# Optimization experiments

Hardware: AMD Instinct MI355X
Metric: run time of the kernel (lower is better)

The kernel has to match this reference:

```python
import jax, jax.numpy as jnp
import numpy as np

N_NODES = 50000
N_EDGES = 800000
N_FEAT = 256
HIDDEN = 64
N_CLASSES = 16
T_END = 3.0  # opt['time']; rk4 takes one step over [0, 3]


def spline_conv(x, src, dst, p, W, R, b, n):
    """SplineConv, dim=1, kernel_size=2, degree=1 open B-spline, aggr='mean'.
    x: [n, Cin]; src/dst: [E]; p: [E,1] pseudo-coords in [0,1];
    W: [2, Cin, Cout]; R: [Cin, Cout]; b: [Cout]."""
    xj = x[src]  # gather source node features [E, Cin]
    # basis weights for K=2, degree=1: (1-p) on kernel 0, p on kernel 1
    msg = ((1.0 - p) * xj) @ W[0] + (p * xj) @ W[1]  # [E, Cout]
    agg = jax.ops.segment_sum(msg, dst, num_segments=n)
    deg = jax.ops.segment_sum(jnp.ones((msg.shape[0], 1), msg.dtype), dst, num_segments=n)
    return agg / jnp.maximum(deg, 1.0) + x @ R + b


def setup_inputs() -> dict:
    key = jax.random.key(0)
    ks = jax.random.split(key, 20)
    x = jax.random.normal(ks[0], (N_NODES, N_FEAT), jnp.float32)
    edge_attr = jax.random.uniform(ks[1], (N_EDGES, 1), jnp.float32)
    src = jax.random.randint(ks[2], (N_EDGES,), 0, N_NODES)
    dst = jax.random.randint(ks[3], (N_EDGES,), 0, N_NODES)

    def w(k, shape, fan_in):
        s = 1.0 / np.sqrt(fan_in)
        return jax.random.uniform(k, shape, jnp.float32, -s, s)

    # conv1: num_features -> hidden
    W1 = w(ks[4], (2, N_FEAT, HIDDEN), N_FEAT)
    R1 = w(ks[5], (N_FEAT, HIDDEN), N_FEAT)
    b1 = jnp.zeros((HIDDEN,), jnp.float32)
    # ODE func: two stacked SplineConvs hidden -> hidden
    Wa = w(ks[6], (2, HIDDEN, HIDDEN), HIDDEN)
    Ra = w(ks[7], (HIDDEN, HIDDEN), HIDDEN)
    ba = jnp.zeros((HIDDEN,), jnp.float32)
    Wb = w(ks[8], (2, HIDDEN, HIDDEN), HIDDEN)
    Rb = w(ks[9], (HIDDEN, HIDDEN), HIDDEN)
    bb = jnp.zeros((HIDDEN,), jnp.float32)
    # conv2: hidden -> num_classes
    W2 = w(ks[10], (2, HIDDEN, N_CLASSES), HIDDEN)
    R2 = w(ks[11], (HIDDEN, N_CLASSES), HIDDEN)
    b2 = jnp.zeros((N_CLASSES,), jnp.float32)

    return dict(x=x, edge_attr=edge_attr, src=src, dst=dst,
                W1=W1, R1=R1, b1=b1, Wa=Wa, Ra=Ra, ba=ba,
                Wb=Wb, Rb=Rb, bb=bb, W2=W2, R2=R2, b2=b2)


def reference(x, edge_attr, src, dst, W1, R1, b1, Wa, Ra, ba, Wb, Rb, bb, W2, R2, b2):
    n = x.shape[0]
    p = edge_attr
    h = jnp.tanh(spline_conv(x, src, dst, p, W1, R1, b1, n))
    # dropout is identity in eval mode

    def f(y):  # GCNLayer: two stacked SplineConvs, no activation
        y = spline_conv(y, src, dst, p, Wa, Ra, ba, n)
        return spline_conv(y, src, dst, p, Wb, Rb, bb, n)

    # single RK4 step from t=0 to t=T_END (torchdiffeq fixed-grid rk4 on s_span=[0,3])
    k1 = f(h)
    k2 = f(h + 0.5 * T_END * k1)
    k3 = f(h + 0.5 * T_END * k2)
    k4 = f(h + T_END * k3)
    h = h + (T_END / 6.0) * (k1 + 2.0 * k2 + 2.0 * k3 + k4)

    out = jnp.tanh(spline_conv(h, src, dst, p, W2, R2, b2, n))
    return jax.nn.log_softmax(out, axis=1)
```

## Files before the change

kernel.cpp:

```cpp
#include <hip/hip_runtime.h>
#include <math.h>

static inline int ceil_div(int a, int b) { return (a + b - 1) / b; }


__global__ __launch_bounds__(256) void zero2(int* __restrict__ a, int* __restrict__ b,
                                             int n) {
    int i = blockIdx.x * 256 + threadIdx.x;
    if (i < n) { a[i] = 0; b[i] = 0; }
}

__global__ __launch_bounds__(256) void hist_kernel(const int* __restrict__ dst,
                                                   int* __restrict__ deg, int E) {
    int e = blockIdx.x * 256 + threadIdx.x;
    if (e < E) atomicAdd(&deg[dst[e]], 1);
}

__global__ __launch_bounds__(256) void scan_blocksum(const int* __restrict__ deg,
                                                     int* __restrict__ bsum, int n) {
    __shared__ int red[256];
    int t = threadIdx.x;
    int base = blockIdx.x * 2048 + t * 8;
    int s = 0;
    #pragma unroll
    for (int i = 0; i < 8; ++i) {
        int idx = base + i;
        if (idx < n) s += deg[idx];
    }
    red[t] = s;
    __syncthreads();
    #pragma unroll
    for (int off = 128; off >= 1; off >>= 1) {
        if (t < off) red[t] += red[t + off];
        __syncthreads();
    }
    if (t == 0) bsum[blockIdx.x] = red[0];
}

__global__ __launch_bounds__(256) void scan_tops(int* __restrict__ bsum, int nb) {
    __shared__ int sh[256];
    int t = threadIdx.x;
    int orig = (t < nb) ? bsum[t] : 0;
    sh[t] = orig;
    __syncthreads();
    for (int off = 1; off < 256; off <<= 1) {
        int add = (t >= off) ? sh[t - off] : 0;
        __syncthreads();
        sh[t] += add;
        __syncthreads();
    }
    if (t < nb) bsum[t] = sh[t] - orig;
}

__global__ __launch_bounds__(256) void scan_final(const int* __restrict__ deg,
                                                  const int* __restrict__ bsum,
                                                  int* __restrict__ rowp,
                                                  float* __restrict__ invd,
                                                  int n, int E) {
    __shared__ int sh[256];
    int t = threadIdx.x;
    int base = blockIdx.x * 2048 + t * 8;
    int loc[8];
    int s = 0;
    #pragma unroll
    for (int i = 0; i < 8; ++i) {
        int idx = base + i;
        int d = (idx < n) ? deg[idx] : 0;
        loc[i] = d;
        s += d;
    }
    sh[t] = s;
    __syncthreads();
    for (int off = 1; off < 256; off <<= 1) {
        int add = (t >= off) ? sh[t - off] : 0;
        __syncthreads();
        sh[t] += add;
        __syncthreads();
    }
    int run = bsum[blockIdx.x] + (sh[t] - s);
    #pragma unroll
    for (int i = 0; i < 8; ++i) {
        int idx = base + i;
        if (idx < n) {
            rowp[idx] = run;
            int d = loc[i];
            run += d;
            invd[idx] = 1.0f / (float)(d > 1 ? d : 1);
        }
    }
    if (blockIdx.x == 0 && t == 0) rowp[n] = E;
}

__global__ __launch_bounds__(256) void scatter_idx(const int* __restrict__ dst,
                                                   const int* __restrict__ rowp,
                                                   int* __restrict__ fill,
                                                   int* __restrict__ ei, int E) {
    int e = blockIdx.x * 256 + threadIdx.x;
    if (e >= E) return;
    int d = dst[e];
    int pos = rowp[d] + atomicAdd(&fill[d], 1);
    ei[pos] = e;
}

__global__ __launch_bounds__(256) void sort_fill(const int* __restrict__ rowp,
                                                 int* __restrict__ ei,
                                                 const int* __restrict__ src,
                                                 const float* __restrict__ p,
                                                 int* __restrict__ es,
                                                 float* __restrict__ ep, int n) {
    int node = blockIdx.x * 256 + threadIdx.x;
    if (node >= n) return;
    int b = rowp[node], e = rowp[node + 1];
    for (int i = b + 1; i < e; ++i) {
        int key = ei[i];
        int j = i - 1;
        while (j >= b && ei[j] > key) { ei[j + 1] = ei[j]; --j; }
        ei[j + 1] = key;
    }
    for (int i = b; i < e; ++i) {
        int id = ei[i];
        es[i] = src[id];
        ep[i] = p[id];
    }
}

__global__ __launch_bounds__(256) void pack_all(
    const float* __restrict__ W1, const float* __restrict__ R1,
    const float* __restrict__ Wa, const float* __restrict__ Ra,
    const float* __restrict__ Wb, const float* __restrict__ Rb,
    const float* __restrict__ W2, const float* __restrict__ R2,
    float* __restrict__ Bc1, float* __restrict__ Bca,
    float* __restrict__ Bcb, float* __restrict__ Bc2) {
    int idx = blockIdx.x * 256 + threadIdx.x;
    const int S1 = 256 * 192, S2 = 192 * 64, S4 = 64 * 48;
    if (idx < S1) {
        int k = idx / 192, c = idx % 192;
        float v;
        if (c < 64)       v = W1[k * 64 + c];
        else if (c < 128) v = W1[256 * 64 + k * 64 + (c - 64)];
        else              v = R1[k * 64 + (c - 128)];
        Bc1[idx] = v;
        return;
    }
    idx -= S1;
    if (idx < S2) { Bca[idx] = (idx < 8192) ? Wa[idx] : Ra[idx - 8192]; return; }
    idx -= S2;
    if (idx < S2) { Bcb[idx] = (idx < 8192) ? Wb[idx] : Rb[idx - 8192]; return; }
    idx -= S2;
    if (idx < S4) {
        int k = idx / 48, c = idx % 48;
        float v;
        if (c < 16)      v = W2[k * 16 + c];
        else if (c < 32) v = W2[64 * 16 + k * 16 + (c - 16)];
        else             v = R2[k * 16 + (c - 32)];
        Bc2[idx] = v;
    }
}

__global__ __launch_bounds__(256) void edge_agg64_v4(const float* __restrict__ x,
                                                     const int* __restrict__ rowp,
                                                     const int* __restrict__ es,
                                                     const float* __restrict__ ep,
                                                     const float* __restrict__ invd,
                                                     float* __restrict__ agg, int n) {
    int gid = blockIdx.x * 256 + threadIdx.x;
    int node = gid >> 4;
    if (node >= n) return;
    int c4 = (gid & 15) << 2;
    int e = rowp[node], eend = rowp[node + 1];
    float sx = 0.f, sy = 0.f, sz = 0.f, sw = 0.f;
    float px = 0.f, py = 0.f, pz = 0.f, pw = 0.f;
    for (; e + 4 <= eend; e += 4) {
        int s0 = es[e], s1 = es[e + 1], s2 = es[e + 2], s3 = es[e + 3];
        float p0 = ep[e], p1 = ep[e + 1], p2 = ep[e + 2], p3 = ep[e + 3];
        float4 v0 = *reinterpret_cast<const float4*>(&x[(size_t)s0 * 64 + c4]);
        float4 v1 = *reinterpret_cast<const float4*>(&x[(size_t)s1 * 64 + c4]);
        float4 v2 = *reinterpret_cast<const float4*>(&x[(size_t)s2 * 64 + c4]);
        float4 v3 = *reinterpret_cast<const float4*>(&x[(size_t)s3 * 64 + c4]);
        sx += (v0.x + v1.x) + (v2.x + v3.x);
        sy += (v0.y + v1.y) + (v2.y + v3.y);
        sz += (v0.z + v1.z) + (v2.z + v3.z);
        sw += (v0.w + v1.w) + (v2.w + v3.w);
        px = fmaf(p0, v0.x, fmaf(p1, v1.x, fmaf(p2, v2.x, fmaf(p3, v3.x, px))));
        py = fmaf(p0, v0.y, fmaf(p1, v1.y, fmaf(p2, v2.y, fmaf(p3, v3.y, py))));
        pz = fmaf(p0, v0.z, fmaf(p1, v1.z, fmaf(p2, v2.z, fmaf(p3, v3.z, pz))));
        pw = fmaf(p0, v0.w, fmaf(p1, v1.w, fmaf(p2, v2.w, fmaf(p3, v3.w, pw))));
    }
    for (; e < eend; ++e) {
        int s = es[e];
        float pe = ep[e];
        float4 v = *reinterpret_cast<const float4*>(&x[(size_t)s * 64 + c4]);
        sx += v.x; sy += v.y; sz += v.z; sw += v.w;
        px = fmaf(pe, v.x, px); py = fmaf(pe, v.y, py);
        pz = fmaf(pe, v.z, pz); pw = fmaf(pe, v.w, pw);
    }
    float w = invd[node];
    float4 a0 = make_float4((sx - px) * w, (sy - py) * w, (sz - pz) * w, (sw - pw) * w);
    float4 a1 = make_float4(px * w, py * w, pz * w, pw * w);
    *reinterpret_cast<float4*>(&agg[(size_t)node * 128 + c4]) = a0;
    *reinterpret_cast<float4*>(&agg[(size_t)node * 128 + 64 + c4]) = a1;
}

__global__ __launch_bounds__(256) void hidden_gemm_db(
    const float* __restrict__ agg, const float* __restrict__ in,
    const float* __restrict__ B, const float* __restrict__ bias,
    int n, int mode, float* __restrict__ u_out,
    const float* __restrict__ hbuf, const float* __restrict__ acc_in,
    float* __restrict__ acc_out, float* __restrict__ t_out,
    float c1, float c2, float c3) {
    __shared__ __align__(16) float As[2][16][68];
    __shared__ __align__(16) float Bs[2][16][68];
    const int t = threadIdx.x;
    const int row0 = blockIdx.x * 64;
    const int ty = t >> 4, tx = t & 15;
    const int lrow = t >> 2, lk = (t & 3) << 2;
    const int bkk = t >> 4, bcol = (t & 15) << 2;

    float4 av = make_float4(0.f, 0.f, 0.f, 0.f);
    {
        int r = row0 + lrow;
        if (r < n) av = *reinterpret_cast<const float4*>(&agg[(size_t)r * 128 + lk]);
    }
    float4 bv = *reinterpret_cast<const float4*>(&B[(size_t)bkk * 64 + bcol]);
    As[0][lk + 0][lrow] = av.x; As[0][lk + 1][lrow] = av.y;
    As[0][lk + 2][lrow] = av.z; As[0][lk + 3][lrow] = av.w;
    *reinterpret_cast<float4*>(&Bs[0][bkk][bcol]) = bv;
    __syncthreads();

    float acc[4][4];
    #pragma unroll
    for (int i = 0; i < 4; ++i)
        #pragma unroll
        for (int j = 0; j < 4; ++j) acc[i][j] = 0.f;

    for (int kt = 0; kt < 12; ++kt) {
        const int cur = kt & 1;
        if (kt + 1 < 12) {
            int k0 = (kt + 1) << 4;
            int r = row0 + lrow;
            int kk = k0 + lk;
            av = make_float4(0.f, 0.f, 0.f, 0.f);
            if (r < n)
                av = (kk < 128)
                    ? *reinterpret_cast<const float4*>(&agg[(size_t)r * 128 + kk])
                    : *reinterpret_cast<const float4*>(&in[(size_t)r * 64 + (kk - 128)]);
            bv = *reinterpret_cast<const float4*>(&B[(size_t)(k0 + bkk) * 64 + bcol]);
        }
        #pragma unroll
        for (int kk = 0; kk < 16; ++kk) {
            float4 a4 = *reinterpret_cast<const float4*>(&As[cur][kk][ty << 2]);
            float4 b4 = *reinterpret_cast<const float4*>(&Bs[cur][kk][tx << 2]);
            float aa[4] = {a4.x, a4.y, a4.z, a4.w};
            float bb[4] = {b4.x, b4.y, b4.z, b4.w};
            #pragma unroll
            for (int i = 0; i < 4; ++i)
                #pragma unroll
                for (int j = 0; j < 4; ++j)
                    acc[i][j] = fmaf(aa[i], bb[j], acc[i][j]);
        }
        if (kt + 1 < 12) {
            const int nx = cur ^ 1;
            As[nx][lk + 0][lrow] = av.x; As[nx][lk + 1][lrow] = av.y;
            As[nx][lk + 2][lrow] = av.z; As[nx][lk + 3][lrow] = av.w;
            *reinterpret_cast<float4*>(&Bs[nx][bkk][bcol]) = bv;
        }
        __syncthreads();
    }

    float4 bia = *reinterpret_cast<const float4*>(&bias[tx << 2]);
    #pragma unroll
    for (int i = 0; i < 4; ++i) {
        int r = row0 + (ty << 2) + i;
        if (r >= n) continue;
        size_t idx = (size_t)r * 64 + (tx << 2);
        float4 v = make_float4(acc[i][0] + bia.x, acc[i][1] + bia.y,
                               acc[i][2] + bia.z, acc[i][3] + bia.w);
        if (mode == 0) {
            *reinterpret_cast<float4*>(&u_out[idx]) = v;
        } else {
            float4 ai = make_float4(0.f, 0.f, 0.f, 0.f);
            if (acc_in) ai = *reinterpret_cast<const float4*>(&acc_in[idx]);
            float4 an = make_float4(ai.x + c3 * v.x, ai.y + c3 * v.y,
                                    ai.z + c3 * v.z, ai.w + c3 * v.w);
            *reinterpret_cast<float4*>(&acc_out[idx]) = an;
            float4 hb = *reinterpret_cast<const float4*>(&hbuf[idx]);
            float4 to = make_float4(hb.x + c1 * v.x + c2 * an.x,
                                    hb.y + c1 * v.y + c2 * an.y,
                                    hb.z + c1 * v.z + c2 * an.z,
                                    hb.w + c1 * v.w + c2 * an.w);
            *reinterpret_cast<float4*>(&t_out[idx]) = to;
        }
    }
}

__global__ __launch_bounds__(128) void conv1_gemm_v3(const float* __restrict__ x,
                                                     const float* __restrict__ B,
                                                     int n, float* __restrict__ yz,
                                                     float* __restrict__ base,
                                                     const float* __restrict__ b1) {
    __shared__ __align__(16) float As[16][68];
    __shared__ __align__(16) float Bs[16][200];
    const int t = threadIdx.x;
    const int row0 = blockIdx.x * 64;
    const int ty = t >> 4, tx = t & 15;
    const int bkk0 = t >> 4, bcol = (t & 15) << 2;
    float acc[8][12];
    #pragma unroll
    for (int i = 0; i < 8; ++i)
        #pragma unroll
        for (int j = 0; j < 12; ++j) acc[i][j] = 0.f;

    for (int kt = 0; kt < 16; ++kt) {
        int k0 = kt << 4;
        #pragma unroll
        for (int hh = 0; hh < 2; ++hh) {
            int q = t + 128 * hh;
            int row = q >> 2;
            int lkq = (q & 3) << 2;
            float4 av = make_float4(0.f, 0.f, 0.f, 0.f);
            int r = row0 + row;
            if (r < n)
                av = *reinterpret_cast<const float4*>(&x[(size_t)r * 256 + k0 + lkq]);
            As[lkq + 0][row] = av.x; As[lkq + 1][row] = av.y;
            As[lkq + 2][row] = av.z; As[lkq + 3][row] = av.w;
        }
        #pragma unroll
        for (int hh = 0; hh < 2; ++hh) {
            int kk = bkk0 + 8 * hh;
            const float* bp = &B[(size_t)(k0 + kk) * 192 + bcol];
            *reinterpret_cast<float4*>(&Bs[kk][bcol])       = *reinterpret_cast<const float4*>(bp);
            *reinterpret_cast<float4*>(&Bs[kk][bcol + 64])  = *reinterpret_cast<const float4*>(bp + 64);
            *reinterpret_cast<float4*>(&Bs[kk][bcol + 128]) = *reinterpret_cast<const float4*>(bp + 128);
        }
        __syncthreads();
        #pragma unroll
        for (int kk = 0; kk < 16; ++kk) {
            float4 a0 = *reinterpret_cast<const float4*>(&As[kk][ty << 3]);
            float4 a1 = *reinterpret_cast<const float4*>(&As[kk][(ty << 3) + 4]);
            float4 b0 = *reinterpret_cast<const float4*>(&Bs[kk][tx << 2]);
            float4 b1q = *reinterpret_cast<const float4*>(&Bs[kk][(tx << 2) + 64]);
            float4 b2q = *reinterpret_cast<const float4*>(&Bs[kk][(tx << 2) + 128]);
            float aa[8] = {a0.x, a0.y, a0.z, a0.w, a1.x, a1.y, a1.z, a1.w};
            float bb[12] = {b0.x, b0.y, b0.z, b0.w, b1q.x, b1q.y, b1q.z, b1q.w,
                            b2q.x, b2q.y, b2q.z, b2q.w};
            #pragma unroll
            for (int i = 0; i < 8; ++i)
                #pragma unroll
                for (int j = 0; j < 12; ++j)
                    acc[i][j] = fmaf(aa[i], bb[j], acc[i][j]);
        }
        __syncthreads();
    }

    float4 bb4 = *reinterpret_cast<const float4*>(&b1[tx << 2]);
    #pragma unroll
    for (int i = 0; i < 8; ++i) {
        int r = row0 + (ty << 3) + i;
        if (r >= n) continue;
        float4 q0 = make_float4(acc[i][0], acc[i][1], acc[i][2], acc[i][3]);
        float4 q1 = make_float4(acc[i][4], acc[i][5], acc[i][6], acc[i][7]);
        float4 q2 = make_float4(acc[i][8] + bb4.x, acc[i][9] + bb4.y,
                                acc[i][10] + bb4.z, acc[i][11] + bb4.w);
        *reinterpret_cast<float4*>(&yz[(size_t)r * 128 + (tx << 2)]) = q0;
        *reinterpret_cast<float4*>(&yz[(size_t)r * 128 + 64 + (tx << 2)]) = q1;
        *reinterpret_cast<float4*>(&base[(size_t)r * 64 + (tx << 2)]) = q2;
    }
}

__global__ __launch_bounds__(256) void edge_tf64_v8(const float* __restrict__ yz,
                                                    const int* __restrict__ rowp,
                                                    const int* __restrict__ es,
                                                    const float* __restrict__ ep,
                                                    const float* __restrict__ invd,
                                                    const float* __restrict__ base,
                                                    float* __restrict__ out, int n) {
    int gid = blockIdx.x * 256 + threadIdx.x;
    int node = gid >> 3;
    if (node >= n) return;
    int c8 = (gid & 7) << 3;
    int e = rowp[node], eend = rowp[node + 1];
    float a[8] = {0.f, 0.f, 0.f, 0.f, 0.f, 0.f, 0.f, 0.f};
    for (; e + 2 <= eend; e += 2) {
        int s0 = es[e], s1 = es[e + 1];
        float p0 = ep[e], p1 = ep[e + 1];
        float4 y0a = *reinterpret_cast<const float4*>(&yz[(size_t)s0 * 128 + c8]);
        float4 y0b = *reinterpret_cast<const float4*>(&yz[(size_t)s0 * 128 + c8 + 4]);
        float4 z0a = *reinterpret_cast<const float4*>(&yz[(size_t)s0 * 128 + 64 + c8]);
        float4 z0b = *reinterpret_cast<const float4*>(&yz[(size_t)s0 * 128 + 64 + c8 + 4]);
        float4 y1a = *reinterpret_cast<const float4*>(&yz[(size_t)s1 * 128 + c8]);
        float4 y1b = *reinterpret_cast<const float4*>(&yz[(size_t)s1 * 128 + c8 + 4]);
        float4 z1a = *reinterpret_cast<const float4*>(&yz[(size_t)s1 * 128 + 64 + c8]);
        float4 z1b = *reinterpret_cast<const float4*>(&yz[(size_t)s1 * 128 + 64 + c8 + 4]);
        const float* ya0 = &y0a.x; const float* yb0 = &y0b.x;
        const float* za0 = &z0a.x; const float* zb0 = &z0b.x;
        const float* ya1 = &y1a.x; const float* yb1 = &y1b.x;
        const float* za1 = &z1a.x; const float* zb1 = &z1b.x;
        #pragma unroll
        for (int j = 0; j < 4; ++j) {
            a[j]     += fmaf(p0, za0[j] - ya0[j], ya0[j]) + fmaf(p1, za1[j] - ya1[j], ya1[j]);
            a[4 + j] += fmaf(p0, zb0[j] - yb0[j], yb0[j]) + fmaf(p1, zb1[j] - yb1[j], yb1[j]);
        }
    }
    for (; e < eend; ++e) {
        int s = es[e];
        float pe = ep[e];
        float4 ya = *reinterpret_cast<const float4*>(&yz[(size_t)s * 128 + c8]);
        float4 yb = *reinterpret_cast<const float4*>(&yz[(size_t)s * 128 + c8 + 4]);
        float4 za = *reinterpret_cast<const float4*>(&yz[(size_t)s * 128 + 64 + c8]);
        float4 zb = *reinterpret_cast<const float4*>(&yz[(size_t)s * 128 + 64 + c8 + 4]);
        const float* fy = &ya.x; const float* gy = &yb.x;
        const float* fz = &za.x; const float* gz = &zb.x;
        #pragma unroll
        for (int j = 0; j < 4; ++j) {
            a[j]     += fmaf(pe, fz[j] - fy[j], fy[j]);
            a[4 + j] += fmaf(pe, gz[j] - gy[j], gy[j]);
        }
    }
    float w = invd[node];
    size_t idx = (size_t)node * 64 + c8;
    float4 ba = *reinterpret_cast<const float4*>(&base[idx]);
    float4 bbv = *reinterpret_cast<const float4*>(&base[idx + 4]);
    float4 o0 = make_float4(tanhf(fmaf(a[0], w, ba.x)), tanhf(fmaf(a[1], w, ba.y)),
                            tanhf(fmaf(a[2], w, ba.z)), tanhf(fmaf(a[3], w, ba.w)));
    float4 o1 = make_float4(tanhf(fmaf(a[4], w, bbv.x)), tanhf(fmaf(a[5], w, bbv.y)),
                            tanhf(fmaf(a[6], w, bbv.z)), tanhf(fmaf(a[7], w, bbv.w)));
    *reinterpret_cast<float4*>(&out[idx]) = o0;
    *reinterpret_cast<float4*>(&out[idx + 4]) = o1;
}

__global__ __launch_bounds__(256) void edge_tf16_lsm(const float* __restrict__ yz,
                                                     const int* __restrict__ rowp,
                                                     const int* __restrict__ es,
                                                     const float* __restrict__ ep,
                                                     const float* __restrict__ invd,
                                                     const float* __restrict__ base,
                                                     float* __restrict__ out, int n) {
    int gid = blockIdx.x * 256 + threadIdx.x;
    int node = gid >> 4;
    if (node >= n) return;
    int c = gid & 15;
    int e = rowp[node], eend = rowp[node + 1];
    float a = 0.f;
    for (; e + 4 <= eend; e += 4) {
        int s0 = es[e], s1 = es[e + 1], s2 = es[e + 2], s3 = es[e + 3];
        float p0 = ep[e], p1 = ep[e + 1], p2 = ep[e + 2], p3 = ep[e + 3];
        float y0 = yz[(size_t)s0 * 32 + c],      z0 = yz[(size_t)s0 * 32 + 16 + c];
        float y1 = yz[(size_t)s1 * 32 + c],      z1 = yz[(size_t)s1 * 32 + 16 + c];
        float y2 = yz[(size_t)s2 * 32 + c],      z2 = yz[(size_t)s2 * 32 + 16 + c];
        float y3 = yz[(size_t)s3 * 32 + c],      z3 = yz[(size_t)s3 * 32 + 16 + c];
        a += fmaf(p0, z0 - y0, y0);
        a += fmaf(p1, z1 - y1, y1);
        a += fmaf(p2, z2 - y2, y2);
        a += fmaf(p3, z3 - y3, y3);
    }
    for (; e < eend; ++e) {
        int s = es[e]; float pe = ep[e];
        float y = yz[(size_t)s * 32 + c], z = yz[(size_t)s * 32 + 16 + c];
        a += fmaf(pe, z - y, y);
    }
    float o = tanhf(a * invd[node] + base[(size_t)node * 16 + c]);
    float m = o;
    #pragma unroll
    for (int off = 8; off >= 1; off >>= 1) m = fmaxf(m, __shfl_xor(m, off, 16));
    float ex = expf(o - m);
    float s = ex;
    #pragma unroll
    for (int off = 8; off >= 1; off >>= 1) s += __shfl_xor(s, off, 16);
    out[(size_t)node * 16 + c] = (o - m) - logf(s);
}

__global__ __launch_bounds__(256) void gemm_tiled(
    const float* __restrict__ A0, int lda0, int K0,
    const float* __restrict__ A1, int lda1,
    const float* __restrict__ B,
    int n, int K, int M,
    float* __restrict__ out0, int w0, const float* __restrict__ bias0,
    float* __restrict__ out1, int w1, const float* __restrict__ bias1,
    int split) {
    __shared__ __align__(16) float As[16][68];
    __shared__ __align__(16) float Bs[16][68];
    const int t = threadIdx.x;
    const int row0 = blockIdx.x * 64;
    const int col0 = blockIdx.y * 64;
    const int ty = t >> 4, tx = t & 15;
    const int lrow = t >> 2, lk = (t & 3) << 2;
    const int bkk = t >> 4, bcol = (t & 15) << 2;
    float acc[4][4];
    #pragma unroll
    for (int i = 0; i < 4; ++i)
        #pragma unroll
        for (int j = 0; j < 4; ++j) acc[i][j] = 0.f;

    for (int k0 = 0; k0 < K; k0 += 16) {
        float4 av = make_float4(0.f, 0.f, 0.f, 0.f);
        {
            int r = row0 + lrow;
            if (r < n) {
                int kk = k0 + lk;
                const float* src = (kk < K0)
                    ? (A0 + (size_t)r * lda0 + kk)
                    : (A1 + (size_t)r * lda1 + (kk - K0));
                av = *reinterpret_cast<const float4*>(src);
            }
        }
        float4 bv = make_float4(0.f, 0.f, 0.f, 0.f);
        {
            int c = col0 + bcol;
            int kk = k0 + bkk;
            if (c < M) bv = *reinterpret_cast<const float4*>(B + (size_t)kk * M + c);
        }
        As[lk + 0][lrow] = av.x; As[lk + 1][lrow] = av.y;
        As[lk + 2][lrow] = av.z; As[lk + 3][lrow] = av.w;
        *reinterpret_cast<float4*>(&Bs[bkk][bcol]) = bv;
        __syncthreads();
        #pragma unroll
        for (int kk = 0; kk < 16; ++kk) {
            float4 a4 = *reinterpret_cast<const float4*>(&As[kk][ty << 2]);
            float4 b4 = *reinterpret_cast<const float4*>(&Bs[kk][tx << 2]);
            float aa[4] = {a4.x, a4.y, a4.z, a4.w};
            float bb[4] = {b4.x, b4.y, b4.z, b4.w};
            #pragma unroll
            for (int i = 0; i < 4; ++i)
                #pragma unroll
                for (int j = 0; j < 4; ++j)
                    acc[i][j] = fmaf(aa[i], bb[j], acc[i][j]);
        }
        __syncthreads();
    }

    #pragma unroll
    for (int i = 0; i < 4; ++i) {
        int r = row0 + (ty << 2) + i;
        if (r >= n) continue;
        #pragma unroll
        for (int j = 0; j < 4; ++j) {
            int c = col0 + (tx << 2) + j;
            if (c >= M) continue;
            float v = acc[i][j];
            if (c < split) {
                if (bias0) v += bias0[c];
                out0[(size_t)r * w0 + c] = v;
            } else {
                int cc = c - split;
                if (bias1) v += bias1[cc];
                out1[(size_t)r * w1 + cc] = v;
            }
        }
    }
}


static void hidden_conv(hipStream_t stream, const float* in, float* agg,
                        const int* rowp, const int* es, const float* ep,
                        const float* invd, const float* Bc, const float* bias, int n,
                        int mode, float* u_out,
                        const float* h, const float* acc_in, float* acc_out,
                        float* t_out, float c1, float c2, float c3) {
    edge_agg64_v4<<<ceil_div(n * 16, 256), 256, 0, stream>>>(in, rowp, es, ep, invd,
                                                             agg, n);
    hidden_gemm_db<<<ceil_div(n, 64), 256, 0, stream>>>(agg, in, Bc, bias, n, mode,
                                                        u_out, h, acc_in, acc_out,
                                                        t_out, c1, c2, c3);
}

extern "C" void kernel_launch(void* const* d_in, const int* in_sizes, int n_in,
                              void* d_out, int out_size, void* d_ws, size_t ws_size,
                              hipStream_t stream) {
    const float* x  = (const float*)d_in[0];
    const float* pE = (const float*)d_in[1];
    const int*   sr = (const int*)d_in[2];
    const int*   ds = (const int*)d_in[3];
    const float* W1 = (const float*)d_in[4];
    const float* R1 = (const float*)d_in[5];
    const float* b1 = (const float*)d_in[6];
    const float* Wa = (const float*)d_in[7];
    const float* Ra = (const float*)d_in[8];
    const float* ba = (const float*)d_in[9];
    const float* Wb = (const float*)d_in[10];
    const float* Rb = (const float*)d_in[11];
    const float* bb = (const float*)d_in[12];
    const float* W2 = (const float*)d_in[13];
    const float* R2 = (const float*)d_in[14];
    const float* b2 = (const float*)d_in[15];
    const int n = in_sizes[0] / 256;
    const int E = in_sizes[2];
    float* out = (float*)d_out;

    char* w = (char*)d_ws;
    auto alloc = [&](size_t bytes) -> void* {
        void* ptr = (void*)w;
        w += (bytes + 255) & ~(size_t)255;
        return ptr;
    };
    int nscan = ceil_div(n, 2048);
    int*   deg  = (int*)alloc((size_t)n * 4);
    int*   fill = (int*)alloc((size_t)n * 4);
    int*   rowp = (int*)alloc((size_t)(n + 1) * 4);
    float* invd = (float*)alloc((size_t)n * 4);
    int*   bsum = (int*)alloc((size_t)256 * 4);
    int*   ei   = (int*)alloc((size_t)E * 4);
    int*   es   = (int*)alloc((size_t)E * 4);
    float* ep   = (float*)alloc((size_t)E * 4);
    float* Bc1  = (float*)alloc((size_t)256 * 192 * 4);
    float* Bca  = (float*)alloc((size_t)192 * 64 * 4);
    float* Bcb  = (float*)alloc((size_t)192 * 64 * 4);
    float* Bc2  = (float*)alloc((size_t)64 * 48 * 4);
    float* big0 = (float*)alloc((size_t)n * 128 * 4);
    float* big1 = (float*)alloc((size_t)n * 64 * 4);
    float* h    = (float*)alloc((size_t)n * 64 * 4);
    float* u    = (float*)alloc((size_t)n * 64 * 4);
    float* tb   = (float*)alloc((size_t)n * 64 * 4);
    float* acc  = (float*)alloc((size_t)n * 64 * 4);

    const int PACK_TOTAL = 256 * 192 + 2 * 192 * 64 + 64 * 48;

    zero2<<<ceil_div(n, 256), 256, 0, stream>>>(deg, fill, n);
    pack_all<<<ceil_div(PACK_TOTAL, 256), 256, 0, stream>>>(W1, R1, Wa, Ra, Wb, Rb,
                                                            W2, R2, Bc1, Bca, Bcb, Bc2);
    hist_kernel<<<ceil_div(E, 256), 256, 0, stream>>>(ds, deg, E);
    scan_blocksum<<<nscan, 256, 0, stream>>>(deg, bsum, n);
    scan_tops<<<1, 256, 0, stream>>>(bsum, nscan);
    scan_final<<<nscan, 256, 0, stream>>>(deg, bsum, rowp, invd, n, E);
    scatter_idx<<<ceil_div(E, 256), 256, 0, stream>>>(ds, rowp, fill, ei, E);
    sort_fill<<<ceil_div(n, 256), 256, 0, stream>>>(rowp, ei, sr, pE, es, ep, n);

    conv1_gemm_v3<<<ceil_div(n, 64), 128, 0, stream>>>(x, Bc1, n, big0, big1, b1);
    edge_tf64_v8<<<ceil_div(n * 8, 256), 256, 0, stream>>>(big0, rowp, es, ep, invd,
                                                           big1, h, n);

    hidden_conv(stream, h, big0, rowp, es, ep, invd, Bca, ba, n, 0, u,
                nullptr, nullptr, nullptr, nullptr, 0.f, 0.f, 0.f);
    hidden_conv(stream, u, big0, rowp, es, ep, invd, Bcb, bb, n, 1, nullptr,
                h, nullptr, acc, tb, 1.5f, 0.f, 1.f);
    hidden_conv(stream, tb, big0, rowp, es, ep, invd, Bca, ba, n, 0, u,
                nullptr, nullptr, nullptr, nullptr, 0.f, 0.f, 0.f);
    hidden_conv(stream, u, big0, rowp, es, ep, invd, Bcb, bb, n, 1, nullptr,
                h, acc, acc, tb, 1.5f, 0.f, 2.f);
    hidden_conv(stream, tb, big0, rowp, es, ep, invd, Bca, ba, n, 0, u,
                nullptr, nullptr, nullptr, nullptr, 0.f, 0.f, 0.f);
    hidden_conv(stream, u, big0, rowp, es, ep, invd, Bcb, bb, n, 1, nullptr,
                h, acc, acc, tb, 3.f, 0.f, 2.f);
    hidden_conv(stream, tb, big0, rowp, es, ep, invd, Bca, ba, n, 0, u,
                nullptr, nullptr, nullptr, nullptr, 0.f, 0.f, 0.f);
    hidden_conv(stream, u, big0, rowp, es, ep, invd, Bcb, bb, n, 1, nullptr,
                h, acc, acc, tb, 0.f, 0.5f, 1.f);

    gemm_tiled<<<dim3(ceil_div(n, 64), 1), 256, 0, stream>>>(
        tb, 64, 64, nullptr, 0, Bc2, n, 64, 48,
        big0, 32, nullptr, big1, 16, b2, 32);
    edge_tf16_lsm<<<ceil_div(n * 16, 256), 256, 0, stream>>>(big0, rowp, es, ep, invd,
                                                             big1, out, n);
}
```

Measured before the change: 878.9 us.

## Fuse setup kernels, deepen edge-gather unrolling, and retile conv1 GEMM for more threads

Merges the zeroing and weight-packing kernels into one grid-stride launch to save a launch. Adds deeper unrolled paths (8 edges, or 4 for the 128-wide gather) to the edge aggregation kernels so more independent gather loads are in flight. Changes the conv1 GEMM from 128 threads with 8x12 register tiles to 256 threads with 4x12 tiles, cutting per-thread registers to raise occupancy at the cost of less register reuse per thread.

```diff
diff --git a/kernel.cpp b/kernel.cpp
--- a/kernel.cpp
+++ b/kernel.cpp
@@ -4,10 +4,42 @@
 static inline int ceil_div(int a, int b) { return (a + b - 1) / b; }
 
 
-__global__ __launch_bounds__(256) void zero2(int* __restrict__ a, int* __restrict__ b,
-                                             int n) {
-    int i = blockIdx.x * 256 + threadIdx.x;
-    if (i < n) { a[i] = 0; b[i] = 0; }
+__global__ __launch_bounds__(256) void setup_zero_pack(
+    int* __restrict__ deg, int* __restrict__ fill, int n,
+    const float* __restrict__ W1, const float* __restrict__ R1,
+    const float* __restrict__ Wa, const float* __restrict__ Ra,
+    const float* __restrict__ Wb, const float* __restrict__ Rb,
+    const float* __restrict__ W2, const float* __restrict__ R2,
+    float* __restrict__ Bc1, float* __restrict__ Bca,
+    float* __restrict__ Bcb, float* __restrict__ Bc2) {
+    int gid = blockIdx.x * 256 + threadIdx.x;
+    int gstride = gridDim.x * 256;
+    for (int i = gid; i < n; i += gstride) { deg[i] = 0; fill[i] = 0; }
+    const int S1 = 256 * 192, S2 = 192 * 64, S4 = 64 * 48;
+    const int TOT = S1 + 2 * S2 + S4;
+    for (int i0 = gid; i0 < TOT; i0 += gstride) {
+        int idx = i0;
+        if (idx < S1) {
+            int k = idx / 192, c = idx % 192;
+            float v;
+            if (c < 64)       v = W1[k * 64 + c];
+            else if (c < 128) v = W1[256 * 64 + k * 64 + (c - 64)];
+            else              v = R1[k * 64 + (c - 128)];
+            Bc1[idx] = v;
+            continue;
+        }
+        idx -= S1;
+        if (idx < S2) { Bca[idx] = (idx < 8192) ? Wa[idx] : Ra[idx - 8192]; continue; }
+        idx -= S2;
+        if (idx < S2) { Bcb[idx] = (idx < 8192) ? Wb[idx] : Rb[idx - 8192]; continue; }
+        idx -= S2;
+        int k = idx / 48, c = idx % 48;
+        float v;
+        if (c < 16)      v = W2[k * 16 + c];
+        else if (c < 32) v = W2[64 * 16 + k * 16 + (c - 16)];
+        else             v = R2[k * 16 + (c - 32)];
+        Bc2[idx] = v;
+    }
 }
 
 __global__ __launch_bounds__(256) void hist_kernel(const int* __restrict__ dst,
@@ -124,40 +156,7 @@
     }
 }
 
-__global__ __launch_bounds__(256) void pack_all(
-    const float* __restrict__ W1, const float* __restrict__ R1,
-    const float* __restrict__ Wa, const float* __restrict__ Ra,
-    const float* __restrict__ Wb, const float* __restrict__ Rb,
-    const float* __restrict__ W2, const float* __restrict__ R2,
-    float* __restrict__ Bc1, float* __restrict__ Bca,
-    float* __restrict__ Bcb, float* __restrict__ Bc2) {
-    int idx = blockIdx.x * 256 + threadIdx.x;
-    const int S1 = 256 * 192, S2 = 192 * 64, S4 = 64 * 48;
-    if (idx < S1) {
-        int k = idx / 192, c = idx % 192;
-        float v;
-        if (c < 64)       v = W1[k * 64 + c];
-        else if (c < 128) v = W1[256 * 64 + k * 64 + (c - 64)];
-        else              v = R1[k * 64 + (c - 128)];
-        Bc1[idx] = v;
-        return;
-    }
-    idx -= S1;
-    if (idx < S2) { Bca[idx] = (idx < 8192) ? Wa[idx] : Ra[idx - 8192]; return; }
-    idx -= S2;
-    if (idx < S2) { Bcb[idx] = (idx < 8192) ? Wb[idx] : Rb[idx - 8192]; return; }
-    idx -= S2;
-    if (idx < S4) {
-        int k = idx / 48, c = idx % 48;
-        float v;
-        if (c < 16)      v = W2[k * 16 + c];
-        else if (c < 32) v = W2[64 * 16 + k * 16 + (c - 16)];
-        else             v = R2[k * 16 + (c - 32)];
-        Bc2[idx] = v;
-    }
-}
-
-__global__ __launch_bounds__(256) void edge_agg64_v4(const float* __restrict__ x,
+__global__ __launch_bounds__(256) void edge_agg64_u8(const float* __restrict__ x,
                                                      const int* __restrict__ rowp,
                                                      const int* __restrict__ es,
                                                      const float* __restrict__ ep,
@@ -170,6 +169,36 @@
     int e = rowp[node], eend = rowp[node + 1];
     float sx = 0.f, sy = 0.f, sz = 0.f, sw = 0.f;
     float px = 0.f, py = 0.f, pz = 0.f, pw = 0.f;
+    for (; e + 8 <= eend; e += 8) {
+        int s0 = es[e], s1 = es[e + 1], s2 = es[e + 2], s3 = es[e + 3];
+        int s4 = es[e + 4], s5 = es[e + 5], s6 = es[e + 6], s7 = es[e + 7];
+        float p0 = ep[e], p1 = ep[e + 1], p2 = ep[e + 2], p3 = ep[e + 3];
+        float p4 = ep[e + 4], p5 = ep[e + 5], p6 = ep[e + 6], p7 = ep[e + 7];
+        float4 v0 = *reinterpret_cast<const float4*>(&x[(size_t)s0 * 64 + c4]);
+        float4 v1 = *reinterpret_cast<const float4*>(&x[(size_t)s1 * 64 + c4]);
+        float4 v2 = *reinterpret_cast<const float4*>(&x[(size_t)s2 * 64 + c4]);
+        float4 v3 = *reinterpret_cast<const float4*>(&x[(size_t)s3 * 64 + c4]);
+        float4 v4 = *reinterpret_cast<const float4*>(&x[(size_t)s4 * 64 + c4]);
+        float4 v5 = *reinterpret_cast<const float4*>(&x[(size_t)s5 * 64 + c4]);
+        float4 v6 = *reinterpret_cast<const float4*>(&x[(size_t)s6 * 64 + c4]);
+        float4 v7 = *reinterpret_cast<const float4*>(&x[(size_t)s7 * 64 + c4]);
+        sx += (v0.x + v1.x) + (v2.x + v3.x);
+        sy += (v0.y + v1.y) + (v2.y + v3.y);
+        sz += (v0.z + v1.z) + (v2.z + v3.z);
+        sw += (v0.w + v1.w) + (v2.w + v3.w);
+        px = fmaf(p0, v0.x, fmaf(p1, v1.x, fmaf(p2, v2.x, fmaf(p3, v3.x, px))));
+        py = fmaf(p0, v0.y, fmaf(p1, v1.y, fmaf(p2, v2.y, fmaf(p3, v3.y, py))));
+        pz = fmaf(p0, v0.z, fmaf(p1, v1.z, fmaf(p2, v2.z, fmaf(p3, v3.z, pz))));
+        pw = fmaf(p0, v0.w, fmaf(p1, v1.w, fmaf(p2, v2.w, fmaf(p3, v3.w, pw))));
+        sx += (v4.x + v5.x) + (v6.x + v7.x);
+        sy += (v4.y + v5.y) + (v6.y + v7.y);
+        sz += (v4.z + v5.z) + (v6.z + v7.z);
+        sw += (v4.w + v5.w) + (v6.w + v7.w);
+        px = fmaf(p4, v4.x, fmaf(p5, v5.x, fmaf(p6, v6.x, fmaf(p7, v7.x, px))));
+        py = fmaf(p4, v4.y, fmaf(p5, v5.y, fmaf(p6, v6.y, fmaf(p7, v7.y, py))));
+        pz = fmaf(p4, v4.z, fmaf(p5, v5.z, fmaf(p6, v6.z, fmaf(p7, v7.z, pz))));
+        pw = fmaf(p4, v4.w, fmaf(p5, v5.w, fmaf(p6, v6.w, fmaf(p7, v7.w, pw))));
+    }
     for (; e + 4 <= eend; e += 4) {
         int s0 = es[e], s1 = es[e + 1], s2 = es[e + 2], s3 = es[e + 3];
         float p0 = ep[e], p1 = ep[e + 1], p2 = ep[e + 2], p3 = ep[e + 3];
@@ -293,58 +322,47 @@
     }
 }
 
-__global__ __launch_bounds__(128) void conv1_gemm_v3(const float* __restrict__ x,
-                                                     const float* __restrict__ B,
-                                                     int n, float* __restrict__ yz,
-                                                     float* __restrict__ base,
-                                                     const float* __restrict__ b1) {
+__global__ __launch_bounds__(256) void conv1_gemm(const float* __restrict__ x,
+                                                  const float* __restrict__ B,
+                                                  int n, float* __restrict__ yz,
+                                                  float* __restrict__ base,
+                                                  const float* __restrict__ b1) {
     __shared__ __align__(16) float As[16][68];
     __shared__ __align__(16) float Bs[16][200];
     const int t = threadIdx.x;
     const int row0 = blockIdx.x * 64;
     const int ty = t >> 4, tx = t & 15;
-    const int bkk0 = t >> 4, bcol = (t & 15) << 2;
-    float acc[8][12];
-    #pragma unroll
-    for (int i = 0; i < 8; ++i)
+    const int lrow = t >> 2, lk = (t & 3) << 2;
+    const int bkk = t >> 4, bcol = (t & 15) << 2;
+    float acc[4][12];
+    #pragma unroll
+    for (int i = 0; i < 4; ++i)
         #pragma unroll
         for (int j = 0; j < 12; ++j) acc[i][j] = 0.f;
 
     for (int kt = 0; kt < 16; ++kt) {
         int k0 = kt << 4;
-        #pragma unroll
-        for (int hh = 0; hh < 2; ++hh) {
-            int q = t + 128 * hh;
-            int row = q >> 2;
-            int lkq = (q & 3) << 2;
-            float4 av = make_float4(0.f, 0.f, 0.f, 0.f);
-            int r = row0 + row;
-            if (r < n)
-                av = *reinterpret_cast<const float4*>(&x[(size_t)r * 256 + k0 + lkq]);
-            As[lkq + 0][row] = av.x; As[lkq + 1][row] = av.y;
-            As[lkq + 2][row] = av.z; As[lkq + 3][row] = av.w;
-        }
-        #pragma unroll
-        for (int hh = 0; hh < 2; ++hh) {
-            int kk = bkk0 + 8 * hh;
-            const float* bp = &B[(size_t)(k0 + kk) * 192 + bcol];
-            *reinterpret_cast<float4*>(&Bs[kk][bcol])       = *reinterpret_cast<const float4*>(bp);
-            *reinterpret_cast<float4*>(&Bs[kk][bcol + 64])  = *reinterpret_cast<const float4*>(bp + 64);
-            *reinterpret_cast<float4*>(&Bs[kk][bcol + 128]) = *reinterpret_cast<const float4*>(bp + 128);
-        }
+        float4 av = make_float4(0.f, 0.f, 0.f, 0.f);
+        int r = row0 + lrow;
+        if (r < n) av = *reinterpret_cast<const float4*>(&x[(size_t)r * 256 + k0 + lk]);
+        As[lk + 0][lrow] = av.x; As[lk + 1][lrow] = av.y;
+        As[lk + 2][lrow] = av.z; As[lk + 3][lrow] = av.w;
+        const float* bp = &B[(size_t)(k0 + bkk) * 192 + bcol];
+        *reinterpret_cast<float4*>(&Bs[bkk][bcol])       = *reinterpret_cast<const float4*>(bp);
+        *reinterpret_cast<float4*>(&Bs[bkk][bcol + 64])  = *reinterpret_cast<const float4*>(bp + 64);
+        *reinterpret_cast<float4*>(&Bs[bkk][bcol + 128]) = *reinterpret_cast<const float4*>(bp + 128);
         __syncthreads();
         #pragma unroll
         for (int kk = 0; kk < 16; ++kk) {
-            float4 a0 = *reinterpret_cast<const float4*>(&As[kk][ty << 3]);
-            float4 a1 = *reinterpret_cast<const float4*>(&As[kk][(ty << 3) + 4]);
+            float4 a4 = *reinterpret_cast<const float4*>(&As[kk][ty << 2]);
             float4 b0 = *reinterpret_cast<const float4*>(&Bs[kk][tx << 2]);
-            float4 b1q = *reinterpret_cast<const float4*>(&Bs[kk][(tx << 2) + 64]);
-            float4 b2q = *reinterpret_cast<const float4*>(&Bs[kk][(tx << 2) + 128]);
-            float aa[8] = {a0.x, a0.y, a0.z, a0.w, a1.x, a1.y, a1.z, a1.w};
-            float bb[12] = {b0.x, b0.y, b0.z, b0.w, b1q.x, b1q.y, b1q.z, b1q.w,
-                            b2q.x, b2q.y, b2q.z, b2q.w};
+            float4 b1v = *reinterpret_cast<const float4*>(&Bs[kk][(tx << 2) + 64]);
+            float4 b2v = *reinterpret_cast<const float4*>(&Bs[kk][(tx << 2) + 128]);
+            float aa[4] = {a4.x, a4.y, a4.z, a4.w};
+            float bb[12] = {b0.x, b0.y, b0.z, b0.w, b1v.x, b1v.y, b1v.z, b1v.w,
+                            b2v.x, b2v.y, b2v.z, b2v.w};
             #pragma unroll
-            for (int i = 0; i < 8; ++i)
+            for (int i = 0; i < 4; ++i)
                 #pragma unroll
                 for (int j = 0; j < 12; ++j)
                     acc[i][j] = fmaf(aa[i], bb[j], acc[i][j]);
@@ -354,8 +372,8 @@
 
     float4 bb4 = *reinterpret_cast<const float4*>(&b1[tx << 2]);
     #pragma unroll
-    for (int i = 0; i < 8; ++i) {
-        int r = row0 + (ty << 3) + i;
+    for (int i = 0; i < 4; ++i) {
+        int r = row0 + (ty << 2) + i;
         if (r >= n) continue;
         float4 q0 = make_float4(acc[i][0], acc[i][1], acc[i][2], acc[i][3]);
         float4 q1 = make_float4(acc[i][4], acc[i][5], acc[i][6], acc[i][7]);
@@ -367,7 +385,7 @@
     }
 }
 
-__global__ __launch_bounds__(256) void edge_tf64_v8(const float* __restrict__ yz,
+__global__ __launch_bounds__(256) void edge_tf64_u4(const float* __restrict__ yz,
                                                     const int* __restrict__ rowp,
                                                     const int* __restrict__ es,
                                                     const float* __restrict__ ep,
@@ -380,6 +398,44 @@
     int c8 = (gid & 7) << 3;
     int e = rowp[node], eend = rowp[node + 1];
     float a[8] = {0.f, 0.f, 0.f, 0.f, 0.f, 0.f, 0.f, 0.f};
+    for (; e + 4 <= eend; e += 4) {
+        int s0 = es[e], s1 = es[e + 1], s2 = es[e + 2], s3 = es[e + 3];
+        float p0 = ep[e], p1 = ep[e + 1], p2 = ep[e + 2], p3 = ep[e + 3];
+        float4 y0a = *reinterpret_cast<const float4*>(&yz[(size_t)s0 * 128 + c8]);
+        float4 y0b = *reinterpret_cast<const float4*>(&yz[(size_t)s0 * 128 + c8 + 4]);
+        float4 z0a = *reinterpret_cast<const float4*>(&yz[(size_t)s0 * 128 + 64 + c8]);
+        float4 z0b = *reinterpret_cast<const float4*>(&yz[(size_t)s0 * 128 + 64 + c8 + 4]);
+        float4 y1a = *reinterpret_cast<const float4*>(&yz[(size_t)s1 * 128 + c8]);
+        float4 y1b = *reinterpret_cast<const float4*>(&yz[(size_t)s1 * 128 + c8 + 4]);
+        float4 z1a = *reinterpret_cast<const float4*>(&yz[(size_t)s1 * 128 + 64 + c8]);
+        float4 z1b = *reinterpret_cast<const float4*>(&yz[(size_t)s1 * 128 + 64 + c8 + 4]);
+        float4 y2a = *reinterpret_cast<const float4*>(&yz[(size_t)s2 * 128 + c8]);
+        float4 y2b = *reinterpret_cast<const float4*>(&yz[(size_t)s2 * 128 + c8 + 4]);
+        float4 z2a = *reinterpret_cast<const float4*>(&yz[(size_t)s2 * 128 + 64 + c8]);
+        float4 z2b = *reinterpret_cast<const float4*>(&yz[(size_t)s2 * 128 + 64 + c8 + 4]);
+        float4 y3a = *reinterpret_cast<const float4*>(&yz[(size_t)s3 * 128 + c8]);
+        float4 y3b = *reinterpret_cast<const float4*>(&yz[(size_t)s3 * 128 + c8 + 4]);
+        float4 z3a = *reinterpret_cast<const float4*>(&yz[(size_t)s3 * 128 + 64 + c8]);
+        float4 z3b = *reinterpret_cast<const float4*>(&yz[(size_t)s3 * 128 + 64 + c8 + 4]);
+        const float* fy0 = &y0a.x; const float* gy0 = &y0b.x;
+        const float* fz0 = &z0a.x; const float* gz0 = &z0b.x;
+        const float* fy1 = &y1a.x; const float* gy1 = &y1b.x;
+        const float* fz1 = &z1a.x; const float* gz1 = &z1b.x;
+        const float* fy2 = &y2a.x; const float* gy2 = &y2b.x;
+        const float* fz2 = &z2a.x; const float* gz2 = &z2b.x;
+        const float* fy3 = &y3a.x; const float* gy3 = &y3b.x;
+        const float* fz3 = &z3a.x; const float* gz3 = &z3b.x;
+        #pragma unroll
+        for (int j = 0; j < 4; ++j) {
+            a[j]     += fmaf(p0, fz0[j] - fy0[j], fy0[j]) + fmaf(p1, fz1[j] - fy1[j], fy1[j]);
+            a[4 + j] += fmaf(p0, gz0[j] - gy0[j], gy0[j]) + fmaf(p1, gz1[j] - gy1[j], gy1[j]);
+        }
+        #pragma unroll
+        for (int j = 0; j < 4; ++j) {
+            a[j]     += fmaf(p2, fz2[j] - fy2[j], fy2[j]) + fmaf(p3, fz3[j] - fy3[j], fy3[j]);
+            a[4 + j] += fmaf(p2, gz2[j] - gy2[j], gy2[j]) + fmaf(p3, gz3[j] - gy3[j], gy3[j]);
+        }
+    }
     for (; e + 2 <= eend; e += 2) {
         int s0 = es[e], s1 = es[e + 1];
         float p0 = ep[e], p1 = ep[e + 1];
@@ -441,13 +497,35 @@
     int c = gid & 15;
     int e = rowp[node], eend = rowp[node + 1];
     float a = 0.f;
+    for (; e + 8 <= eend; e += 8) {
+        int s0 = es[e], s1 = es[e + 1], s2 = es[e + 2], s3 = es[e + 3];
+        int s4 = es[e + 4], s5 = es[e + 5], s6 = es[e + 6], s7 = es[e + 7];
+        float p0 = ep[e], p1 = ep[e + 1], p2 = ep[e + 2], p3 = ep[e + 3];
+        float p4 = ep[e + 4], p5 = ep[e + 5], p6 = ep[e + 6], p7 = ep[e + 7];
+        float y0 = yz[(size_t)s0 * 32 + c], z0 = yz[(size_t)s0 * 32 + 16 + c];
+        float y1 = yz[(size_t)s1 * 32 + c], z1 = yz[(size_t)s1 * 32 + 16 + c];
+        float y2 = yz[(size_t)s2 * 32 + c], z2 = yz[(size_t)s2 * 32 + 16 + c];
+        float y3 = yz[(size_t)s3 * 32 + c], z3 = yz[(size_t)s3 * 32 + 16 + c];
+        float y4 = yz[(size_t)s4 * 32 + c], z4 = yz[(size_t)s4 * 32 + 16 + c];
+        float y5 = yz[(size_t)s5 * 32 + c], z5 = yz[(size_t)s5 * 32 + 16 + c];
+        float y6 = yz[(size_t)s6 * 32 + c], z6 = yz[(size_t)s6 * 32 + 16 + c];
+        float y7 = yz[(size_t)s7 * 32 + c], z7 = yz[(size_t)s7 * 32 + 16 + c];
+        a += fmaf(p0, z0 - y0, y0);
+        a += fmaf(p1, z1 - y1, y1);
+        a += fmaf(p2, z2 - y2, y2);
+        a += fmaf(p3, z3 - y3, y3);
+        a += fmaf(p4, z4 - y4, y4);
+        a += fmaf(p5, z5 - y5, y5);
+        a += fmaf(p6, z6 - y6, y6);
+        a += fmaf(p7, z7 - y7, y7);
+    }
     for (; e + 4 <= eend; e += 4) {
         int s0 = es[e], s1 = es[e + 1], s2 = es[e + 2], s3 = es[e + 3];
         float p0 = ep[e], p1 = ep[e + 1], p2 = ep[e + 2], p3 = ep[e + 3];
-        float y0 = yz[(size_t)s0 * 32 + c],      z0 = yz[(size_t)s0 * 32 + 16 + c];
-        float y1 = yz[(size_t)s1 * 32 + c],      z1 = yz[(size_t)s1 * 32 + 16 + c];
-        float y2 = yz[(size_t)s2 * 32 + c],      z2 = yz[(size_t)s2 * 32 + 16 + c];
-        float y3 = yz[(size_t)s3 * 32 + c],      z3 = yz[(size_t)s3 * 32 + 16 + c];
+        float y0 = yz[(size_t)s0 * 32 + c], z0 = yz[(size_t)s0 * 32 + 16 + c];
+        float y1 = yz[(size_t)s1 * 32 + c], z1 = yz[(size_t)s1 * 32 + 16 + c];
+        float y2 = yz[(size_t)s2 * 32 + c], z2 = yz[(size_t)s2 * 32 + 16 + c];
+        float y3 = yz[(size_t)s3 * 32 + c], z3 = yz[(size_t)s3 * 32 + 16 + c];
         a += fmaf(p0, z0 - y0, y0);
         a += fmaf(p1, z1 - y1, y1);
         a += fmaf(p2, z2 - y2, y2);
@@ -556,7 +634,7 @@
                         int mode, float* u_out,
                         const float* h, const float* acc_in, float* acc_out,
                         float* t_out, float c1, float c2, float c3) {
-    edge_agg64_v4<<<ceil_div(n * 16, 256), 256, 0, stream>>>(in, rowp, es, ep, invd,
+    edge_agg64_u8<<<ceil_div(n * 16, 256), 256, 0, stream>>>(in, rowp, es, ep, invd,
                                                              agg, n);
     hidden_gemm_db<<<ceil_div(n, 64), 256, 0, stream>>>(agg, in, Bc, bias, n, mode,
                                                         u_out, h, acc_in, acc_out,
@@ -612,11 +690,8 @@
     float* tb   = (float*)alloc((size_t)n * 64 * 4);
     float* acc  = (float*)alloc((size_t)n * 64 * 4);
 
-    const int PACK_TOTAL = 256 * 192 + 2 * 192 * 64 + 64 * 48;
-
-    zero2<<<ceil_div(n, 256), 256, 0, stream>>>(deg, fill, n);
-    pack_all<<<ceil_div(PACK_TOTAL, 256), 256, 0, stream>>>(W1, R1, Wa, Ra, Wb, Rb,
-                                                            W2, R2, Bc1, Bca, Bcb, Bc2);
+    setup_zero_pack<<<288, 256, 0, stream>>>(deg, fill, n, W1, R1, Wa, Ra, Wb, Rb,
+                                             W2, R2, Bc1, Bca, Bcb, Bc2);
     hist_kernel<<<ceil_div(E, 256), 256, 0, stream>>>(ds, deg, E);
     scan_blocksum<<<nscan, 256, 0, stream>>>(deg, bsum, n);
     scan_tops<<<1, 256, 0, stream>>>(bsum, nscan);
@@ -624,8 +699,8 @@
     scatter_idx<<<ceil_div(E, 256), 256, 0, stream>>>(ds, rowp, fill, ei, E);
     sort_fill<<<ceil_div(n, 256), 256, 0, stream>>>(rowp, ei, sr, pE, es, ep, n);
 
-    conv1_gemm_v3<<<ceil_div(n, 64), 128, 0, stream>>>(x, Bc1, n, big0, big1, b1);
-    edge_tf64_v8<<<ceil_div(n * 8, 256), 256, 0, stream>>>(big0, rowp, es, ep, invd,
+    conv1_gemm<<<ceil_div(n, 64), 256, 0, stream>>>(x, Bc1, n, big0, big1, b1);
+    edge_tf64_u4<<<ceil_div(n * 8, 256), 256, 0, stream>>>(big0, rowp, es, ep, invd,
                                                            big1, h, n);
 
     hidden_conv(stream, h, big0, rowp, es, ep, invd, Bca, ba, n, 0, u,
```

Result: no change. 884.4 us (+0.6%).
